# Performance work log

Hardware: AMD Instinct MI355X
Metric: run time of the kernel (lower is better)

## Reference

```python
import jax, jax.numpy as jnp
import numpy as np

B, N, K = 4, 2048, 32
CQ, CK, CV = 128, 128, 256
CQ1, CK1 = max(CQ, 32), max(CK, 32)
NUM_GROUPS = 32
EPS = 1e-5


def conv1x1(x, W, b):
    # x: [B,Cin,N,K], W: [Cout,Cin], b: [Cout]
    return jnp.einsum('oc,bcnk->bonk', W, x) + b[None, :, None, None]


def group_norm(x, gamma, beta, num_groups=NUM_GROUPS, eps=EPS):
    # x: [B,C,N,K]; stats over (C//G, N, K) per group, per sample (torch GroupNorm)
    b, c, n, k = x.shape
    xg = x.reshape(b, num_groups, c // num_groups, n, k)
    mean = xg.mean(axis=(2, 3, 4), keepdims=True)
    var = xg.var(axis=(2, 3, 4), keepdims=True)
    xg = (xg - mean) * jax.lax.rsqrt(var + eps)
    x = xg.reshape(b, c, n, k)
    return x * gamma[None, :, None, None] + beta[None, :, None, None]


def setup_inputs() -> dict:
    key = jax.random.key(0)
    ks = jax.random.split(key, 24)
    nrm = lambda k, shape, s=0.05: jax.random.normal(k, shape, jnp.float32) * s
    return {
        'feat': jax.random.normal(ks[0], (B, CQ, N), jnp.float32),
        'grouped_feat': jax.random.normal(ks[1], (B, CK, N, K), jnp.float32),
        'grouped_feat_out': jax.random.normal(ks[2], (B, CV, N, K), jnp.float32),
        'count': jax.random.randint(ks[3], (B, N), 0, K + 1, jnp.int32),
        'W_fc': nrm(ks[4], (CQ1, CQ)), 'b_fc': nrm(ks[5], (CQ1,)),
        'W_gc': nrm(ks[6], (CK1, CK)), 'b_gc': nrm(ks[7], (CK1,)),
        'g1': jnp.ones((CQ1 + CK1,), jnp.float32), 'be1': jnp.zeros((CQ1 + CK1,), jnp.float32),
        'W_w1': nrm(ks[8], (CV, CQ1 + CK1)), 'b_w1': nrm(ks[9], (CV,)),
        'g2': jnp.ones((CV,), jnp.float32), 'be2': jnp.zeros((CV,), jnp.float32),
        'W_w2': nrm(ks[10], (CV, CV)), 'b_w2': nrm(ks[11], (CV,)),
        'W_fo': nrm(ks[12], (CV, CV)), 'b_fo': nrm(ks[13], (CV,)),
        'g3': jnp.ones((CV,), jnp.float32), 'be3': jnp.zeros((CV,), jnp.float32),
    }


def reference(feat, grouped_feat, grouped_feat_out, count,
              W_fc, b_fc, W_gc, b_gc, g1, be1, W_w1, b_w1,
              g2, be2, W_w2, b_w2, W_fo, b_fo, g3, be3):
    # feat_conv (1x1 on [B,CQ,N,1]) then expand along K
    feat1 = jnp.einsum('oc,bcn->bon', W_fc, feat) + b_fc[None, :, None]  # [B,CQ1,N]
    feat1 = jnp.broadcast_to(feat1[..., None], (B, CQ1, N, K))
    gfeat1 = conv1x1(grouped_feat, W_gc, b_gc)  # [B,CK1,N,K]
    total = jnp.concatenate([feat1, gfeat1], axis=1)  # [B,CQ1+CK1,N,K]

    # weight_conv: ReLU -> GN -> Conv -> ReLU -> GN -> Conv
    x = jax.nn.relu(total)
    x = group_norm(x, g1, be1)
    x = conv1x1(x, W_w1, b_w1)
    x = jax.nn.relu(x)
    x = group_norm(x, g2, be2)
    scores = conv1x1(x, W_w2, b_w2)  # [B,CV,N,K]

    # count-based neighbor mask
    cnt = jnp.clip(count, 1, None)
    mask = (jnp.arange(K, dtype=cnt.dtype) < cnt[..., None]).astype(scores.dtype)  # [B,N,K]
    mask = mask[:, None]  # [B,1,N,K]
    scores = scores * mask + (-1e9) * (1.0 - mask)
    weight = jax.nn.softmax(scores, axis=-1)

    # feat_out_conv: Conv -> GN -> ReLU
    gout = conv1x1(grouped_feat_out, W_fo, b_fo)
    gout = jax.nn.relu(group_norm(gout, g3, be3))

    return (gout * weight).sum(axis=-1)  # [B,CV,N]
```

## Files before the change

kernel.cpp:

```cpp
#include <hip/hip_runtime.h>
#include <stdint.h>

#define DEVI __device__ __forceinline__

typedef __attribute__((ext_vector_type(4))) int    i32x4;
typedef __attribute__((ext_vector_type(4))) float  f32x4;
typedef __attribute__((ext_vector_type(8))) __bf16 bf16x8;

static constexpr int BB = 4, NN = 2048, KK = 32, PP = NN * KK;
static constexpr float GEPS = 1e-5f;

DEVI unsigned short f2bf(float f) {
  unsigned u = __builtin_bit_cast(unsigned, f);
  return (unsigned short)((u + 0x7FFFu + ((u >> 16) & 1u)) >> 16);
}
DEVI float bf2f(unsigned short h) {
  unsigned u = (unsigned)h << 16;
  return __builtin_bit_cast(float, u);
}
DEVI uint2 pack4(float a, float b, float c, float d) {
  return make_uint2((unsigned)f2bf(a) | ((unsigned)f2bf(b) << 16),
                    (unsigned)f2bf(c) | ((unsigned)f2bf(d) << 16));
}
DEVI void mfma16(f32x4& d, i32x4 a, i32x4 b) {
  d = __builtin_amdgcn_mfma_f32_16x16x32_bf16(
      __builtin_bit_cast(bf16x8, a), __builtin_bit_cast(bf16x8, b), d, 0, 0, 0);
}

__global__ void prep_kern(const float* Wfc, const float* Wgc, const float* Wfo,
                          unsigned short* dWfc, unsigned short* dWgc, unsigned short* dWfo) {
  int i = blockIdx.x * 256 + threadIdx.x;
  if (i < 16384)       dWfc[i] = f2bf(Wfc[i]);
  else if (i < 32768)  dWgc[i - 16384] = f2bf(Wgc[i - 16384]);
  else if (i < 98304)  dWfo[i - 32768] = f2bf(Wfo[i - 32768]);
}

template<int CIN, int COUT, int MODE, bool RELU>
__global__ __launch_bounds__(512, 4)
void gemm_kern(const void* srcA, const void* srcB,
               const unsigned short* Wmat, const float* bias,
               unsigned short* out, float* stats, int group_base,
               int P, int tiles_per_b, int nblk) {
  constexpr int MW = COUT / 8;
  constexpr int MF = MW / 16;
  constexpr int KS = CIN / 32;
  constexpr int CINP = CIN + 8;
  __shared__ unsigned short tile[64 * CINP];

  const int tid = threadIdx.x;
  const int lane = tid & 63, w = tid >> 6;
  const int l15 = lane & 15, lg = lane >> 4;
  const int b = blockIdx.x / nblk, blk = blockIdx.x % nblk;

  const unsigned short* Wb = (MODE == 1) ? (Wmat + (size_t)b * COUT * CIN) : Wmat;
  const float* biasb = (MODE == 1) ? (bias + b * COUT) : bias;

  i32x4 a[KS][MF];
#pragma unroll
  for (int ks = 0; ks < KS; ++ks)
#pragma unroll
    for (int mf = 0; mf < MF; ++mf)
      a[ks][mf] = *(const i32x4*)(Wb + (size_t)(w * MW + mf * 16 + l15) * CIN + ks * 32 + lg * 8);

  f32x4 bi[MF];
#pragma unroll
  for (int mf = 0; mf < MF; ++mf)
    bi[mf] = *(const f32x4*)(biasb + w * MW + mf * 16 + lg * 4);

  float ssum[MF], ssq[MF];
#pragma unroll
  for (int mf = 0; mf < MF; ++mf) { ssum[mf] = 0.f; ssq[mf] = 0.f; }

  for (int t = blk; t < tiles_per_b; t += nblk) {
    const int p0 = t * 64;
    if (MODE == 0) {
      const float* src = (const float*)srcA + (size_t)b * CIN * P + p0;
      const int cq = tid >> 4, pq = tid & 15;
#pragma unroll
      for (int pass = 0; pass < CIN / 128; ++pass) {
        const int c0 = pass * 128 + cq * 4;
        f32x4 v[4];
#pragma unroll
        for (int i = 0; i < 4; ++i)
          v[i] = *(const f32x4*)(src + (size_t)(c0 + i) * (size_t)P + pq * 4);
#pragma unroll
        for (int jj = 0; jj < 4; ++jj)
          *(uint2*)&tile[(pq * 4 + jj) * CINP + c0] =
              pack4(v[0][jj], v[1][jj], v[2][jj], v[3][jj]);
      }
    } else {
      const unsigned short* r1b = (const unsigned short*)srcA + (size_t)b * NN * 128;
      const unsigned short* r2b = (const unsigned short*)srcB + (size_t)b * PP * 128;
      const int p = tid >> 3;
#pragma unroll
      for (int j = 0; j < 4; ++j) {
        const int chunk = j * 8 + (tid & 7);
        const int c = chunk * 8;
        const unsigned short* sp;
        if (c < 128) {
          const int n = (p0 + p) >> 5;
          sp = r1b + (size_t)n * 128 + c;
        } else {
          sp = r2b + (size_t)(p0 + p) * 128 + (c - 128);
        }
        *(uint4*)&tile[p * CINP + c] = *(const uint4*)sp;
      }
    }
    __syncthreads();

    f32x4 acc[MF][4];
#pragma unroll
    for (int mf = 0; mf < MF; ++mf)
#pragma unroll
      for (int nf = 0; nf < 4; ++nf) acc[mf][nf] = f32x4{0.f, 0.f, 0.f, 0.f};

#pragma unroll
    for (int ks = 0; ks < KS; ++ks) {
      i32x4 b4[4];
#pragma unroll
      for (int nf = 0; nf < 4; ++nf)
        b4[nf] = *(const i32x4*)&tile[(nf * 16 + l15) * CINP + ks * 32 + lg * 8];
#pragma unroll
      for (int mf = 0; mf < MF; ++mf)
#pragma unroll
        for (int nf = 0; nf < 4; ++nf) mfma16(acc[mf][nf], a[ks][mf], b4[nf]);
    }
    __syncthreads();

#pragma unroll
    for (int mf = 0; mf < MF; ++mf) {
      const int o4 = w * MW + mf * 16 + lg * 4;
#pragma unroll
      for (int nf = 0; nf < 4; ++nf) {
        const int p = p0 + nf * 16 + l15;
        float y0 = acc[mf][nf][0] + bi[mf][0];
        float y1 = acc[mf][nf][1] + bi[mf][1];
        float y2 = acc[mf][nf][2] + bi[mf][2];
        float y3 = acc[mf][nf][3] + bi[mf][3];
        if (RELU) {
          y0 = fmaxf(y0, 0.f); y1 = fmaxf(y1, 0.f);
          y2 = fmaxf(y2, 0.f); y3 = fmaxf(y3, 0.f);
        }
        ssum[mf] += y0 + y1 + y2 + y3;
        ssq[mf] += y0 * y0 + y1 * y1 + y2 * y2 + y3 * y3;
        *(uint2*)(out + ((size_t)b * P + p) * COUT + o4) = pack4(y0, y1, y2, y3);
      }
    }
  }

#pragma unroll
  for (int mf = 0; mf < MF; ++mf) {
    float s = ssum[mf], q = ssq[mf];
#pragma unroll
    for (int d = 1; d < 16; d <<= 1) { s += __shfl_xor(s, d); q += __shfl_xor(q, d); }
    if (l15 == 0) {
      int g = group_base + ((w * MW + mf * 16 + lg * 4) >> 3);
      atomicAdd(&stats[(b * 32 + g) * 2 + 0], s);
      atomicAdd(&stats[(b * 32 + g) * 2 + 1], q);
    }
  }
}

__global__ void fold1_kern(const float* st1, const float* g1, const float* be1,
                           const float* W_w1, const float* b_w1,
                           unsigned short* W1p, float* b1p) {
  int b = blockIdx.x, tid = threadIdx.x;
  __shared__ float s_l[256], t_l[256];
  {
    int c = tid, g = c >> 3;
    float cnt = (g < 16) ? (8.f * NN) : (8.f * NN * KK);
    float su = st1[(b * 32 + g) * 2], sq = st1[(b * 32 + g) * 2 + 1];
    float mean = su / cnt;
    float var = fmaxf(sq / cnt - mean * mean, 0.f);
    float s = g1[c] * rsqrtf(var + GEPS);
    s_l[c] = s; t_l[c] = be1[c] - mean * s;
  }
  __syncthreads();
  int o = tid;
  float acc = b_w1[o];
  for (int c4 = 0; c4 < 64; ++c4) {
    float4 wv = *(const float4*)(W_w1 + o * 256 + c4 * 4);
    *(uint2*)&W1p[((size_t)b * 256 + o) * 256 + c4 * 4] =
        pack4(wv.x * s_l[c4 * 4], wv.y * s_l[c4 * 4 + 1],
              wv.z * s_l[c4 * 4 + 2], wv.w * s_l[c4 * 4 + 3]);
    acc += wv.x * t_l[c4 * 4] + wv.y * t_l[c4 * 4 + 1] +
           wv.z * t_l[c4 * 4 + 2] + wv.w * t_l[c4 * 4 + 3];
  }
  b1p[b * 256 + o] = acc;
}

__global__ void fold23_kern(const float* st2, const float* st3,
                            const float* g2, const float* be2,
                            const float* W_w2, const float* b_w2,
                            const float* g3, const float* be3,
                            unsigned short* W2p, float* b2p, float* s3t3) {
  int b = blockIdx.x, tid = threadIdx.x;
  __shared__ float s_l[256], t_l[256];
  {
    int c = tid, g = c >> 3;
    float cnt = 8.f * NN * KK;
    float su = st2[(b * 32 + g) * 2], sq = st2[(b * 32 + g) * 2 + 1];
    float mean = su / cnt;
    float var = fmaxf(sq / cnt - mean * mean, 0.f);
    float s = g2[c] * rsqrtf(var + GEPS);
    s_l[c] = s; t_l[c] = be2[c] - mean * s;

    float su3 = st3[(b * 32 + g) * 2], sq3 = st3[(b * 32 + g) * 2 + 1];
    float mean3 = su3 / cnt;
    float var3 = fmaxf(sq3 / cnt - mean3 * mean3, 0.f);
    float s3 = g3[c] * rsqrtf(var3 + GEPS);
    s3t3[(b * 256 + c) * 2 + 0] = s3;
    s3t3[(b * 256 + c) * 2 + 1] = be3[c] - mean3 * s3;
  }
  __syncthreads();
  int o = tid;
  float acc = b_w2[o];
  for (int c4 = 0; c4 < 64; ++c4) {
    float4 wv = *(const float4*)(W_w2 + o * 256 + c4 * 4);
    *(uint2*)&W2p[((size_t)b * 256 + o) * 256 + c4 * 4] =
        pack4(wv.x * s_l[c4 * 4], wv.y * s_l[c4 * 4 + 1],
              wv.z * s_l[c4 * 4 + 2], wv.w * s_l[c4 * 4 + 3]);
    acc += wv.x * t_l[c4 * 4] + wv.y * t_l[c4 * 4 + 1] +
           wv.z * t_l[c4 * 4 + 2] + wv.w * t_l[c4 * 4 + 3];
  }
  b2p[b * 256 + o] = acc;
}

__global__ __launch_bounds__(512, 4)
void k5_kern(const unsigned short* x2t, const unsigned short* gor,
             const unsigned short* W2p, const float* b2p,
             const float* s3t3, const int* count, float* out, int nblk) {
  constexpr int GP = 264;
  __shared__ unsigned short gt[64 * GP];
  const int tid = threadIdx.x, lane = tid & 63, w = tid >> 6;
  const int l15 = lane & 15, lg = lane >> 4;
  const int b = blockIdx.x / nblk, blk = blockIdx.x % nblk;

  const unsigned short* Wb = W2p + (size_t)b * 65536;

  i32x4 wb[8][2];
#pragma unroll
  for (int ks = 0; ks < 8; ++ks)
#pragma unroll
    for (int of = 0; of < 2; ++of)
      wb[ks][of] = *(const i32x4*)(Wb + (size_t)(w * 32 + of * 16 + l15) * 256 + ks * 32 + lg * 8);

  float bia[2], s3v[2], t3v[2];
#pragma unroll
  for (int of = 0; of < 2; ++of) {
    int o = w * 32 + of * 16 + l15;
    bia[of] = b2p[b * 256 + o];
    s3v[of] = s3t3[(b * 256 + o) * 2 + 0];
    t3v[of] = s3t3[(b * 256 + o) * 2 + 1];
  }

  const unsigned short* xb = x2t + (size_t)b * PP * 256;
  const unsigned short* gb = gor + (size_t)b * PP * 256;

  for (int t = blk; t < 1024; t += nblk) {
    const int p0 = t * 64, n0 = p0 >> 5;

    {
      const unsigned short* gsrc = gb + (size_t)p0 * 256;
      const int p = tid >> 3;
#pragma unroll
      for (int j = 0; j < 4; ++j) {
        const int c = (j * 8 + (tid & 7)) * 8;
        *(uint4*)&gt[p * GP + c] = *(const uint4*)(gsrc + (size_t)p * 256 + c);
      }
    }
    __syncthreads();

    f32x4 acc[4][2];
#pragma unroll
    for (int pf = 0; pf < 4; ++pf)
#pragma unroll
      for (int of = 0; of < 2; ++of) acc[pf][of] = f32x4{0.f, 0.f, 0.f, 0.f};

#pragma unroll
    for (int ks = 0; ks < 8; ++ks) {
      i32x4 af[4];
#pragma unroll
      for (int pf = 0; pf < 4; ++pf)
        af[pf] = *(const i32x4*)(xb + (size_t)(p0 + pf * 16 + l15) * 256 + ks * 32 + lg * 8);
#pragma unroll
      for (int pf = 0; pf < 4; ++pf)
#pragma unroll
        for (int of = 0; of < 2; ++of) mfma16(acc[pf][of], af[pf], wb[ks][of]);
    }

    const int cnt0 = max(count[b * NN + n0], 1);
    const int cnt1 = max(count[b * NN + n0 + 1], 1);
#pragma unroll
    for (int of = 0; of < 2; ++of) {
      const int o = w * 32 + of * 16 + l15;
      float res[2];
#pragma unroll
      for (int pair = 0; pair < 2; ++pair) {
        const int cnt = pair ? cnt1 : cnt0;
        float sc[2][4];
#pragma unroll
        for (int ph = 0; ph < 2; ++ph)
#pragma unroll
          for (int r = 0; r < 4; ++r) {
            int k = ph * 16 + lg * 4 + r;
            float v = acc[pair * 2 + ph][of][r] + bia[of];
            sc[ph][r] = (k < cnt) ? v : -1e9f;
          }
        float m = sc[0][0];
#pragma unroll
        for (int ph = 0; ph < 2; ++ph)
#pragma unroll
          for (int r = 0; r < 4; ++r) m = fmaxf(m, sc[ph][r]);
        m = fmaxf(m, __shfl_xor(m, 16));
        m = fmaxf(m, __shfl_xor(m, 32));
        float den = 0.f, con = 0.f;
#pragma unroll
        for (int ph = 0; ph < 2; ++ph)
#pragma unroll
          for (int r = 0; r < 4; ++r) {
            float e = __expf(sc[ph][r] - m);
            int prel = pair * 32 + ph * 16 + lg * 4 + r;
            float g = bf2f(gt[prel * GP + o]);
            g = fmaxf(s3v[of] * g + t3v[of], 0.f);
            den += e; con += e * g;
          }
        den += __shfl_xor(den, 16); con += __shfl_xor(con, 16);
        den += __shfl_xor(den, 32); con += __shfl_xor(con, 32);
        res[pair] = con / den;
      }
      if (lg == 0)
        *(float2*)(out + (size_t)(b * 256 + o) * NN + n0) = make_float2(res[0], res[1]);
    }
    __syncthreads();
  }
}

extern "C" void kernel_launch(void* const* d_in, const int* in_sizes, int n_in,
                              void* d_out, int out_size, void* d_ws, size_t ws_size,
                              hipStream_t stream) {
  const float* feat = (const float*)d_in[0];
  const float* gf   = (const float*)d_in[1];
  const float* gfo  = (const float*)d_in[2];
  const int*   cnt  = (const int*)d_in[3];
  const float* W_fc = (const float*)d_in[4];
  const float* b_fc = (const float*)d_in[5];
  const float* W_gc = (const float*)d_in[6];
  const float* b_gc = (const float*)d_in[7];
  const float* g1   = (const float*)d_in[8];
  const float* be1  = (const float*)d_in[9];
  const float* W_w1 = (const float*)d_in[10];
  const float* b_w1 = (const float*)d_in[11];
  const float* g2   = (const float*)d_in[12];
  const float* be2  = (const float*)d_in[13];
  const float* W_w2 = (const float*)d_in[14];
  const float* b_w2 = (const float*)d_in[15];
  const float* W_fo = (const float*)d_in[16];
  const float* b_fo = (const float*)d_in[17];
  const float* g3   = (const float*)d_in[18];
  const float* be3  = (const float*)d_in[19];
  float* out = (float*)d_out;
  char* ws = (char*)d_ws;

  constexpr size_t ST1 = 0, ST2 = 1024, ST3 = 2048;
  constexpr size_t WFC = 4096;
  constexpr size_t WGC = WFC + 32768;
  constexpr size_t WFO = WGC + 32768;
  constexpr size_t W1P = WFO + 131072;
  constexpr size_t B1P = W1P + 524288;
  constexpr size_t W2P = B1P + 4096;
  constexpr size_t B2P = W2P + 524288;
  constexpr size_t S3T = B2P + 4096;
  constexpr size_t R1  = 2097152;
  constexpr size_t X2  = R1 + 2097152;
  constexpr size_t R2  = X2 + 134217728;
  constexpr size_t GOR = R2;
  constexpr size_t WS_NEED = GOR + 134217728;
  if (ws_size < WS_NEED) return;

  float* st1 = (float*)(ws + ST1);
  float* st2 = (float*)(ws + ST2);
  float* st3 = (float*)(ws + ST3);
  unsigned short* wfc = (unsigned short*)(ws + WFC);
  unsigned short* wgc = (unsigned short*)(ws + WGC);
  unsigned short* wfo = (unsigned short*)(ws + WFO);
  unsigned short* w1p = (unsigned short*)(ws + W1P);
  float* b1p = (float*)(ws + B1P);
  unsigned short* w2p = (unsigned short*)(ws + W2P);
  float* b2p = (float*)(ws + B2P);
  float* s3t = (float*)(ws + S3T);
  unsigned short* r1 = (unsigned short*)(ws + R1);
  unsigned short* x2 = (unsigned short*)(ws + X2);
  unsigned short* r2 = (unsigned short*)(ws + R2);
  unsigned short* gor = (unsigned short*)(ws + GOR);

  hipMemsetAsync(ws, 0, 3072, stream);
  prep_kern<<<384, 256, 0, stream>>>(W_fc, W_gc, W_fo, wfc, wgc, wfo);

  gemm_kern<128, 128, 0, true><<<dim3(4 * 32), 512, 0, stream>>>(
      feat, nullptr, wfc, b_fc, r1, st1, 0, NN, NN / 64, 32);
  gemm_kern<128, 128, 0, true><<<dim3(4 * 128), 512, 0, stream>>>(
      gf, nullptr, wgc, b_gc, r2, st1, 16, PP, PP / 64, 128);

  fold1_kern<<<4, 256, 0, stream>>>(st1, g1, be1, W_w1, b_w1, w1p, b1p);

  gemm_kern<256, 256, 1, true><<<dim3(4 * 128), 512, 0, stream>>>(
      r1, r2, w1p, b1p, x2, st2, 0, PP, PP / 64, 128);

  gemm_kern<256, 256, 0, false><<<dim3(4 * 128), 512, 0, stream>>>(
      gfo, nullptr, wfo, b_fo, gor, st3, 0, PP, PP / 64, 128);

  fold23_kern<<<4, 256, 0, stream>>>(st2, st3, g2, be2, W_w2, b_w2, g3, be3, w2p, b2p, s3t);

  k5_kern<<<dim3(4 * 128), 512, 0, stream>>>(x2, gor, w2p, b2p, s3t, cnt, out, 128);
}
```

Baseline: 775.0 us.

## Double-buffer LDS tiles with register prefetch and XOR swizzle in GEMM and softmax kernels

Splits the GEMM and final softmax-reduce kernels into a register-prefetch plus double-buffered shared-memory pipeline, so the global loads for the next tile are in flight while the current tile is being computed. One of the two __syncthreads per iteration is removed. The tile size becomes CIN-dependent (32 points for 256-channel inputs), and an XOR swizzle is applied to LDS columns to reduce bank conflicts. The risks are smaller tiles per iteration, more register pressure from the prefetch buffers, and the swizzle and indexing having to stay consistent between the writers and the readers.

```diff
diff --git a/kernel.cpp b/kernel.cpp
--- a/kernel.cpp
+++ b/kernel.cpp
@@ -37,15 +37,18 @@
 
 template<int CIN, int COUT, int MODE, bool RELU>
 __global__ __launch_bounds__(512, 4)
-void gemm_kern(const void* srcA, const void* srcB,
-               const unsigned short* Wmat, const float* bias,
-               unsigned short* out, float* stats, int group_base,
+void gemm_kern(const void* __restrict__ srcA, const void* __restrict__ srcB,
+               const unsigned short* __restrict__ Wmat, const float* __restrict__ bias,
+               unsigned short* __restrict__ out, float* __restrict__ stats, int group_base,
                int P, int tiles_per_b, int nblk) {
-  constexpr int MW = COUT / 8;
-  constexpr int MF = MW / 16;
-  constexpr int KS = CIN / 32;
+  constexpr int TP   = 8192 / CIN;
+  constexpr int NF   = TP / 16;
+  constexpr int MW   = COUT / 8;
+  constexpr int MF   = MW / 16;
+  constexpr int KS   = CIN / 32;
   constexpr int CINP = CIN + 8;
-  __shared__ unsigned short tile[64 * CINP];
+  constexpr int PQN  = TP / 4;
+  __shared__ unsigned short tile[2][TP * CINP];
 
   const int tid = threadIdx.x;
   const int lane = tid & 63, w = tid >> 6;
@@ -71,67 +74,78 @@
 #pragma unroll
   for (int mf = 0; mf < MF; ++mf) { ssum[mf] = 0.f; ssq[mf] = 0.f; }
 
-  for (int t = blk; t < tiles_per_b; t += nblk) {
-    const int p0 = t * 64;
-    if (MODE == 0) {
-      const float* src = (const float*)srcA + (size_t)b * CIN * P + p0;
-      const int cq = tid >> 4, pq = tid & 15;
-#pragma unroll
-      for (int pass = 0; pass < CIN / 128; ++pass) {
-        const int c0 = pass * 128 + cq * 4;
-        f32x4 v[4];
-#pragma unroll
-        for (int i = 0; i < 4; ++i)
-          v[i] = *(const f32x4*)(src + (size_t)(c0 + i) * (size_t)P + pq * 4);
-#pragma unroll
-        for (int jj = 0; jj < 4; ++jj)
-          *(uint2*)&tile[(pq * 4 + jj) * CINP + c0] =
-              pack4(v[0][jj], v[1][jj], v[2][jj], v[3][jj]);
+  const int cq = tid / PQN, pq = tid % PQN;
+  const float* src0 = (const float*)srcA + (size_t)b * CIN * P;
+  const int sp = tid >> 4, st7 = tid & 15;
+  const unsigned short* r1b = (const unsigned short*)srcA + (size_t)b * NN * 128;
+  const unsigned short* r2b = (const unsigned short*)srcB + (size_t)b * PP * 128;
+
+  f32x4 pv0[4];
+  uint4 pv1[2];
+
+  auto issue = [&](int tt) {
+    if constexpr (MODE == 0) {
+      const float* s = src0 + (size_t)tt * TP + pq * 4;
+#pragma unroll
+      for (int i = 0; i < 4; ++i)
+        pv0[i] = *(const f32x4*)(s + (size_t)(cq * 4 + i) * (size_t)P);
+    } else {
+      pv1[0] = *(const uint4*)(r1b + (size_t)tt * 128 + st7 * 8);
+      pv1[1] = *(const uint4*)(r2b + ((size_t)tt * 32 + sp) * 128 + st7 * 8);
+    }
+  };
+  auto stage = [&](int cb) {
+    unsigned short* tl = tile[cb];
+    if constexpr (MODE == 0) {
+#pragma unroll
+      for (int jj = 0; jj < 4; ++jj) {
+        const int row = pq * 4 + jj;
+        const int slot = (((cq >> 1) ^ ((row >> 3) & 3)) * 8 + (cq & 1) * 4);
+        *(uint2*)&tl[row * CINP + slot] =
+            pack4(pv0[0][jj], pv0[1][jj], pv0[2][jj], pv0[3][jj]);
       }
     } else {
-      const unsigned short* r1b = (const unsigned short*)srcA + (size_t)b * NN * 128;
-      const unsigned short* r2b = (const unsigned short*)srcB + (size_t)b * PP * 128;
-      const int p = tid >> 3;
-#pragma unroll
-      for (int j = 0; j < 4; ++j) {
-        const int chunk = j * 8 + (tid & 7);
-        const int c = chunk * 8;
-        const unsigned short* sp;
-        if (c < 128) {
-          const int n = (p0 + p) >> 5;
-          sp = r1b + (size_t)n * 128 + c;
-        } else {
-          sp = r2b + (size_t)(p0 + p) * 128 + (c - 128);
-        }
-        *(uint4*)&tile[p * CINP + c] = *(const uint4*)sp;
+      const int f = (sp >> 3) & 3;
+      *(uint4*)&tl[sp * CINP + ((0 + st7) ^ f) * 8] = pv1[0];
+      *(uint4*)&tl[sp * CINP + ((16 + st7) ^ f) * 8] = pv1[1];
+    }
+  };
+
+  int cb = 0;
+  issue(blk);
+  for (int t = blk; t < tiles_per_b; t += nblk) {
+    stage(cb);
+    if (t + nblk < tiles_per_b) issue(t + nblk);
+    __syncthreads();
+
+    const unsigned short* tl = tile[cb];
+    const int p0 = t * TP;
+
+    f32x4 acc[MF][NF];
+#pragma unroll
+    for (int mf = 0; mf < MF; ++mf)
+#pragma unroll
+      for (int nf = 0; nf < NF; ++nf) acc[mf][nf] = f32x4{0.f, 0.f, 0.f, 0.f};
+
+#pragma unroll
+    for (int ks = 0; ks < KS; ++ks) {
+      i32x4 b4[NF];
+#pragma unroll
+      for (int nf = 0; nf < NF; ++nf) {
+        const int row = nf * 16 + l15;
+        b4[nf] = *(const i32x4*)&tl[row * CINP + (((ks * 4 + lg) ^ ((row >> 3) & 3)) * 8)];
       }
-    }
-    __syncthreads();
-
-    f32x4 acc[MF][4];
-#pragma unroll
-    for (int mf = 0; mf < MF; ++mf)
-#pragma unroll
-      for (int nf = 0; nf < 4; ++nf) acc[mf][nf] = f32x4{0.f, 0.f, 0.f, 0.f};
-
-#pragma unroll
-    for (int ks = 0; ks < KS; ++ks) {
-      i32x4 b4[4];
-#pragma unroll
-      for (int nf = 0; nf < 4; ++nf)
-        b4[nf] = *(const i32x4*)&tile[(nf * 16 + l15) * CINP + ks * 32 + lg * 8];
 #pragma unroll
       for (int mf = 0; mf < MF; ++mf)
 #pragma unroll
-        for (int nf = 0; nf < 4; ++nf) mfma16(acc[mf][nf], a[ks][mf], b4[nf]);
-    }
-    __syncthreads();
+        for (int nf = 0; nf < NF; ++nf) mfma16(acc[mf][nf], a[ks][mf], b4[nf]);
+    }
 
 #pragma unroll
     for (int mf = 0; mf < MF; ++mf) {
       const int o4 = w * MW + mf * 16 + lg * 4;
 #pragma unroll
-      for (int nf = 0; nf < 4; ++nf) {
+      for (int nf = 0; nf < NF; ++nf) {
         const int p = p0 + nf * 16 + l15;
         float y0 = acc[mf][nf][0] + bi[mf][0];
         float y1 = acc[mf][nf][1] + bi[mf][1];
@@ -146,6 +160,7 @@
         *(uint2*)(out + ((size_t)b * P + p) * COUT + o4) = pack4(y0, y1, y2, y3);
       }
     }
+    cb ^= 1;
   }
 
 #pragma unroll
@@ -227,11 +242,12 @@
 }
 
 __global__ __launch_bounds__(512, 4)
-void k5_kern(const unsigned short* x2t, const unsigned short* gor,
-             const unsigned short* W2p, const float* b2p,
-             const float* s3t3, const int* count, float* out, int nblk) {
+void k5_kern(const unsigned short* __restrict__ x2t, const unsigned short* __restrict__ gor,
+             const unsigned short* __restrict__ W2p, const float* __restrict__ b2p,
+             const float* __restrict__ s3t3, const int* __restrict__ count,
+             float* __restrict__ out, int tiles_per_b, int nblk) {
   constexpr int GP = 264;
-  __shared__ unsigned short gt[64 * GP];
+  __shared__ unsigned short gt[2][32 * GP];
   const int tid = threadIdx.x, lane = tid & 63, w = tid >> 6;
   const int l15 = lane & 15, lg = lane >> 4;
   const int b = blockIdx.x / nblk, blk = blockIdx.x % nblk;
@@ -257,82 +273,86 @@
   const unsigned short* xb = x2t + (size_t)b * PP * 256;
   const unsigned short* gb = gor + (size_t)b * PP * 256;
 
-  for (int t = blk; t < 1024; t += nblk) {
-    const int p0 = t * 64, n0 = p0 >> 5;
-
-    {
-      const unsigned short* gsrc = gb + (size_t)p0 * 256;
-      const int p = tid >> 3;
-#pragma unroll
-      for (int j = 0; j < 4; ++j) {
-        const int c = (j * 8 + (tid & 7)) * 8;
-        *(uint4*)&gt[p * GP + c] = *(const uint4*)(gsrc + (size_t)p * 256 + c);
-      }
-    }
+  const int sp = tid >> 4, st7 = tid & 15;
+  uint4 pvg[2];
+  auto issue = [&](int tt) {
+    const unsigned short* g = gb + ((size_t)tt * 32 + sp) * 256;
+    pvg[0] = *(const uint4*)(g + (0 + st7) * 8);
+    pvg[1] = *(const uint4*)(g + (16 + st7) * 8);
+  };
+  auto stage = [&](int cb) {
+    unsigned short* tl = gt[cb];
+    const int f = (sp >> 3) & 3;
+    *(uint4*)&tl[sp * GP + ((0 + st7) ^ f) * 8] = pvg[0];
+    *(uint4*)&tl[sp * GP + ((16 + st7) ^ f) * 8] = pvg[1];
+  };
+
+  int cb = 0;
+  issue(blk);
+  for (int t = blk; t < tiles_per_b; t += nblk) {
+    stage(cb);
+    if (t + nblk < tiles_per_b) issue(t + nblk);
     __syncthreads();
 
-    f32x4 acc[4][2];
-#pragma unroll
-    for (int pf = 0; pf < 4; ++pf)
+    const unsigned short* tl = gt[cb];
+    const int p0 = t * 32;
+
+    f32x4 acc[2][2];
+#pragma unroll
+    for (int pf = 0; pf < 2; ++pf)
 #pragma unroll
       for (int of = 0; of < 2; ++of) acc[pf][of] = f32x4{0.f, 0.f, 0.f, 0.f};
 
 #pragma unroll
     for (int ks = 0; ks < 8; ++ks) {
-      i32x4 af[4];
-#pragma unroll
-      for (int pf = 0; pf < 4; ++pf)
+      i32x4 af[2];
+#pragma unroll
+      for (int pf = 0; pf < 2; ++pf)
         af[pf] = *(const i32x4*)(xb + (size_t)(p0 + pf * 16 + l15) * 256 + ks * 32 + lg * 8);
 #pragma unroll
-      for (int pf = 0; pf < 4; ++pf)
+      for (int pf = 0; pf < 2; ++pf)
 #pragma unroll
         for (int of = 0; of < 2; ++of) mfma16(acc[pf][of], af[pf], wb[ks][of]);
     }
 
-    const int cnt0 = max(count[b * NN + n0], 1);
-    const int cnt1 = max(count[b * NN + n0 + 1], 1);
+    const int cnt = max(count[b * NN + t], 1);
 #pragma unroll
     for (int of = 0; of < 2; ++of) {
       const int o = w * 32 + of * 16 + l15;
-      float res[2];
-#pragma unroll
-      for (int pair = 0; pair < 2; ++pair) {
-        const int cnt = pair ? cnt1 : cnt0;
-        float sc[2][4];
-#pragma unroll
-        for (int ph = 0; ph < 2; ++ph)
-#pragma unroll
-          for (int r = 0; r < 4; ++r) {
-            int k = ph * 16 + lg * 4 + r;
-            float v = acc[pair * 2 + ph][of][r] + bia[of];
-            sc[ph][r] = (k < cnt) ? v : -1e9f;
-          }
-        float m = sc[0][0];
-#pragma unroll
-        for (int ph = 0; ph < 2; ++ph)
-#pragma unroll
-          for (int r = 0; r < 4; ++r) m = fmaxf(m, sc[ph][r]);
-        m = fmaxf(m, __shfl_xor(m, 16));
-        m = fmaxf(m, __shfl_xor(m, 32));
-        float den = 0.f, con = 0.f;
-#pragma unroll
-        for (int ph = 0; ph < 2; ++ph)
-#pragma unroll
-          for (int r = 0; r < 4; ++r) {
-            float e = __expf(sc[ph][r] - m);
-            int prel = pair * 32 + ph * 16 + lg * 4 + r;
-            float g = bf2f(gt[prel * GP + o]);
-            g = fmaxf(s3v[of] * g + t3v[of], 0.f);
-            den += e; con += e * g;
-          }
-        den += __shfl_xor(den, 16); con += __shfl_xor(con, 16);
-        den += __shfl_xor(den, 32); con += __shfl_xor(con, 32);
-        res[pair] = con / den;
-      }
+      const int o3 = o >> 3, o7 = o & 7;
+      float sc[2][4];
+#pragma unroll
+      for (int pf = 0; pf < 2; ++pf)
+#pragma unroll
+        for (int r = 0; r < 4; ++r) {
+          int k = pf * 16 + lg * 4 + r;
+          float v = acc[pf][of][r] + bia[of];
+          sc[pf][r] = (k < cnt) ? v : -1e9f;
+        }
+      float m = sc[0][0];
+#pragma unroll
+      for (int pf = 0; pf < 2; ++pf)
+#pragma unroll
+        for (int r = 0; r < 4; ++r) m = fmaxf(m, sc[pf][r]);
+      m = fmaxf(m, __shfl_xor(m, 16));
+      m = fmaxf(m, __shfl_xor(m, 32));
+      float den = 0.f, con = 0.f;
+#pragma unroll
+      for (int pf = 0; pf < 2; ++pf)
+#pragma unroll
+        for (int r = 0; r < 4; ++r) {
+          float e = __expf(sc[pf][r] - m);
+          int prel = pf * 16 + lg * 4 + r;
+          float g = bf2f(tl[prel * GP + ((o3 ^ ((prel >> 3) & 3)) * 8 + o7)]);
+          g = fmaxf(s3v[of] * g + t3v[of], 0.f);
+          den += e; con += e * g;
+        }
+      den += __shfl_xor(den, 16); con += __shfl_xor(con, 16);
+      den += __shfl_xor(den, 32); con += __shfl_xor(con, 32);
       if (lg == 0)
-        *(float2*)(out + (size_t)(b * 256 + o) * NN + n0) = make_float2(res[0], res[1]);
-    }
-    __syncthreads();
+        out[(size_t)(b * 256 + o) * NN + t] = con / den;
+    }
+    cb ^= 1;
   }
 }
 
@@ -405,12 +425,12 @@
   fold1_kern<<<4, 256, 0, stream>>>(st1, g1, be1, W_w1, b_w1, w1p, b1p);
 
   gemm_kern<256, 256, 1, true><<<dim3(4 * 128), 512, 0, stream>>>(
-      r1, r2, w1p, b1p, x2, st2, 0, PP, PP / 64, 128);
+      r1, r2, w1p, b1p, x2, st2, 0, PP, PP / 32, 128);
 
   gemm_kern<256, 256, 0, false><<<dim3(4 * 128), 512, 0, stream>>>(
-      gfo, nullptr, wfo, b_fo, gor, st3, 0, PP, PP / 64, 128);
+      gfo, nullptr, wfo, b_fo, gor, st3, 0, PP, PP / 32, 128);
 
   fold23_kern<<<4, 256, 0, stream>>>(st2, st3, g2, be2, W_w2, b_w2, g3, be3, w2p, b2p, s3t);
 
-  k5_kern<<<dim3(4 * 128), 512, 0, stream>>>(x2, gor, w2p, b2p, s3t, cnt, out, 128);
-}
+  k5_kern<<<dim3(4 * 128), 512, 0, stream>>>(x2, gor, w2p, b2p, s3t, cnt, out, PP / 32, 128);
+}
```

Result: slower. 806.3 us (+4.0%).
